# Performance work log

Measured on AMD Instinct MI355X. Metric: run time of the kernel, lower is better.

The kernel has to match this reference:

```python
import jax, jax.numpy as jnp
import numpy as np

D_MODEL = 1024
N_HEAD = 16
HEAD_DIM = D_MODEL // N_HEAD
D_INNER = (int(D_MODEL * 2.0) + 7) // 8 * 8  # 2048
EPS = 1e-6


def setup_inputs() -> dict:
    key = jax.random.key(0)
    ks = jax.random.split(key, 8)
    B, T = 2, 2048
    s = 0.02
    return {
        "x": jax.random.normal(ks[0], (B, T, D_MODEL), dtype=jnp.float32),
        "ln1_w": jnp.ones((D_MODEL,), jnp.float32),
        "ln2_w": jnp.ones((D_MODEL,), jnp.float32),
        "qkv_w": jax.random.normal(ks[1], (3 * D_MODEL, D_MODEL), jnp.float32) * s,
        "o_w": jax.random.normal(ks[2], (D_MODEL, D_MODEL), jnp.float32) * s,
        "gate_w": jax.random.normal(ks[3], (D_INNER, D_MODEL), jnp.float32) * s,
        "up_w": jax.random.normal(ks[4], (D_INNER, D_MODEL), jnp.float32) * s,
        "down_w": jax.random.normal(ks[5], (D_MODEL, D_INNER), jnp.float32) * s,
    }


def _rmsnorm(x, w):
    xf = x.astype(jnp.float32)
    rms = jax.lax.rsqrt(jnp.mean(xf * xf, axis=-1, keepdims=True) + EPS)
    return (xf * rms).astype(x.dtype) * w


def _attention(x, qkv_w, o_w):
    B, T, D = x.shape
    qkv = (x @ qkv_w.T).reshape(B, T, 3, N_HEAD, HEAD_DIM)
    q, k, v = qkv[:, :, 0], qkv[:, :, 1], qkv[:, :, 2]  # [B,T,H,hd]
    scale = 1.0 / np.sqrt(HEAD_DIM)
    att = jnp.einsum("bqhd,bkhd->bhqk", q, k) * scale
    causal = jnp.tril(jnp.ones((T, T), dtype=bool))
    att = jnp.where(causal[None, None], att, -jnp.inf)
    att = jax.nn.softmax(att, axis=-1)
    y = jnp.einsum("bhqk,bkhd->bqhd", att, v).reshape(B, T, D)
    return y @ o_w.T


def _ffn(x, gate_w, up_w, down_w):
    g = jax.nn.silu(x @ gate_w.T)
    u = x @ up_w.T
    return (g * u) @ down_w.T


def reference(x, ln1_w, ln2_w, qkv_w, o_w, gate_w, up_w, down_w):
    x = x + _attention(_rmsnorm(x, ln1_w), qkv_w, o_w)
    x = x + _ffn(_rmsnorm(x, ln2_w), gate_w, up_w, down_w)
    return x
```

## Files before the change

### kernel.cpp

```cpp
#include <hip/hip_runtime.h>
#include <hip/hip_bf16.h>
#include <cstdint>

typedef __hip_bfloat16 bf16;
typedef __attribute__((ext_vector_type(8))) short bf16x8;
typedef __attribute__((ext_vector_type(4))) float f32x4;
typedef __attribute__((ext_vector_type(4))) int i32x4;

#define T_SEQ 2048
#define DMODEL 1024
#define NHEAD 16
#define DHEAD 64
#define MROWS 4096

typedef const __attribute__((address_space(1))) void* gas_ptr;
typedef __attribute__((address_space(3))) void* las_ptr;

static __device__ __forceinline__ f32x4 mfma16(bf16x8 a, bf16x8 b, f32x4 c) {
  return __builtin_amdgcn_mfma_f32_16x16x32_bf16(a, b, c, 0, 0, 0);
}
static __device__ __forceinline__ void gload_lds16(const void* g, void* l) {
  __builtin_amdgcn_global_load_lds((gas_ptr)g, (las_ptr)l, 16, 0, 0);
}
static __device__ __forceinline__ float b2f(unsigned short u) {
  union { unsigned int i; float f; } x; x.i = ((unsigned int)u) << 16; return x.f;
}
static __device__ __forceinline__ unsigned short f2bu(float f) {
  __hip_bfloat16 h = __float2bfloat16(f);
  unsigned short u; __builtin_memcpy(&u, &h, 2); return u;
}

__global__ void f2b_k(const float* __restrict__ in, bf16* __restrict__ out, int n) {
  int idx = (blockIdx.x * blockDim.x + threadIdx.x) * 4;
  if (idx < n) {
    float4 v = *(const float4*)(in + idx);
    out[idx]     = __float2bfloat16(v.x);
    out[idx + 1] = __float2bfloat16(v.y);
    out[idx + 2] = __float2bfloat16(v.z);
    out[idx + 3] = __float2bfloat16(v.w);
  }
}

__global__ __launch_bounds__(256) void rms_k(const float* __restrict__ x,
                                             const float* __restrict__ w,
                                             bf16* __restrict__ out) {
  const int row = blockIdx.x;
  const int tid = threadIdx.x;
  const float4 v = ((const float4*)(x + (size_t)row * DMODEL))[tid];
  float ss = v.x * v.x + v.y * v.y + v.z * v.z + v.w * v.w;
#pragma unroll
  for (int off = 32; off; off >>= 1) ss += __shfl_xor(ss, off);
  __shared__ float red[4];
  if ((tid & 63) == 0) red[tid >> 6] = ss;
  __syncthreads();
  const float tot = red[0] + red[1] + red[2] + red[3];
  const float rinv = rsqrtf(tot * (1.f / DMODEL) + 1e-6f);
  const float4 wv = ((const float4*)w)[tid];
  bf16* o = out + (size_t)row * DMODEL + tid * 4;
  o[0] = __float2bfloat16(v.x * rinv * wv.x);
  o[1] = __float2bfloat16(v.y * rinv * wv.y);
  o[2] = __float2bfloat16(v.z * rinv * wv.z);
  o[3] = __float2bfloat16(v.w * rinv * wv.w);
}

template <int K, int EPI>
__global__ __launch_bounds__(256) void gemm_bt(const bf16* __restrict__ A,
                                               const bf16* __restrict__ Bw, int N,
                                               void* __restrict__ o0, void* __restrict__ o1,
                                               void* __restrict__ o2,
                                               const float* __restrict__ res) {
  __shared__ bf16 As[128 * 32];
  __shared__ bf16 Bs[128 * 32];
  const int bn0 = blockIdx.x * 128;
  const int bm0 = blockIdx.y * 128;
  const int tid = threadIdx.x;
  const int wave = tid >> 6, lane = tid & 63;
  const int wr = wave >> 1, wc = wave & 1;
  const int fr = lane & 15, g8 = (lane >> 4) * 8, r4 = (lane >> 4) * 4;
  const int srow = lane >> 2;
  const int scol = (lane & 3) * 8;

  const f32x4 fzero = {0.f, 0.f, 0.f, 0.f};
  f32x4 acc[4][4];
#pragma unroll
  for (int i = 0; i < 4; i++)
#pragma unroll
    for (int j = 0; j < 4; j++) acc[i][j] = fzero;

  const bf16* gA0 = A + (size_t)(bm0 + wave * 16 + srow) * K + scol;
  const bf16* gA1 = A + (size_t)(bm0 + (wave + 4) * 16 + srow) * K + scol;
  const bf16* gB0 = Bw + (size_t)(bn0 + wave * 16 + srow) * K + scol;
  const bf16* gB1 = Bw + (size_t)(bn0 + (wave + 4) * 16 + srow) * K + scol;

  for (int k0 = 0; k0 < K; k0 += 32) {
    gload_lds16(gA0 + k0, &As[wave * 512]);
    gload_lds16(gA1 + k0, &As[(wave + 4) * 512]);
    gload_lds16(gB0 + k0, &Bs[wave * 512]);
    gload_lds16(gB1 + k0, &Bs[(wave + 4) * 512]);
    __syncthreads();
    bf16x8 af[4], bfr[4];
#pragma unroll
    for (int mr = 0; mr < 4; mr++)
      af[mr] = *(const bf16x8*)&As[(wr * 64 + mr * 16 + fr) * 32 + g8];
#pragma unroll
    for (int nr = 0; nr < 4; nr++)
      bfr[nr] = *(const bf16x8*)&Bs[(wc * 64 + nr * 16 + fr) * 32 + g8];
#pragma unroll
    for (int mr = 0; mr < 4; mr++)
#pragma unroll
      for (int nr = 0; nr < 4; nr++)
        acc[mr][nr] = mfma16(af[mr], bfr[nr], acc[mr][nr]);
    __syncthreads();
  }

#pragma unroll
  for (int mr = 0; mr < 4; mr++) {
#pragma unroll
    for (int nr = 0; nr < 4; nr++) {
#pragma unroll
      for (int r = 0; r < 4; r++) {
        const int row = bm0 + wr * 64 + mr * 16 + r4 + r;
        const int col = bn0 + wc * 64 + nr * 16 + fr;
        const float vsum = acc[mr][nr][r];
        if (EPI == 0) {
          ((bf16*)o0)[(size_t)row * N + col] = __float2bfloat16(vsum);
        } else if (EPI == 1) {
          const int sel = col >> 10;
          const int n = col & 1023;
          const int h = n >> 6, d = n & 63;
          const int b = row >> 11, t = row & 2047;
          if (sel == 2) {
            ((bf16*)o2)[(((size_t)(b * NHEAD + h)) * DHEAD + d) * T_SEQ + t] =
                __float2bfloat16(vsum);
          } else {
            bf16* dst = (sel == 0) ? (bf16*)o0 : (bf16*)o1;
            dst[(((size_t)(b * NHEAD + h)) * T_SEQ + t) * DHEAD + d] = __float2bfloat16(vsum);
          }
        } else if (EPI == 2) {
          ((float*)o0)[(size_t)row * N + col] = res[(size_t)row * N + col] + vsum;
        } else {
          const int half = N >> 1;
          bf16* dst = (col < half) ? (bf16*)o0 : (bf16*)o1;
          const int c = (col < half) ? col : col - half;
          dst[(size_t)row * half + c] = __float2bfloat16(vsum);
        }
      }
    }
  }
}

__global__ __launch_bounds__(256) void attn_k(const bf16* __restrict__ qb,
                                              const bf16* __restrict__ kb,
                                              const bf16* __restrict__ vt,
                                              bf16* __restrict__ y) {
  const int wave = threadIdx.x >> 6, lane = threadIdx.x & 63;
  const int xcd = blockIdx.x & 7;
  const int j = blockIdx.x >> 3;
  const int bh = xcd * 4 + (j & 3);
  const int qt = 31 - (j >> 2);
  const int b = bh >> 4, h = bh & 15;
  const int fr = lane & 15, g8 = (lane >> 4) * 8, r4 = (lane >> 4) * 4;
  const int u = lane >> 4;
  const int src1 = fr + ((u & 1) << 5);
  const int src2 = src1 + 16;
  const bool hB = u >= 2;

  const bf16* qp = qb + (size_t)bh * T_SEQ * DHEAD;
  const bf16* kp = kb + (size_t)bh * T_SEQ * DHEAD;
  const bf16* vp = vt + (size_t)bh * DHEAD * T_SEQ;

  __shared__ char Ks[2][4096];
  __shared__ char Vs[2][4096];

  const int q0 = qt * 64 + wave * 16;
  const int kend = q0 + 16;
  const int qrow = q0 + fr;
  const int nb = 2 * qt + 2;

  const bf16x8 qf0 = *(const bf16x8*)(qp + (size_t)(q0 + fr) * DHEAD + g8);
  const bf16x8 qf1 = *(const bf16x8*)(qp + (size_t)(q0 + fr) * DHEAD + 32 + g8);

  const int krow_l = lane >> 3;
  const int kslot_l = (lane & 7) ^ krow_l;
  const int vrow_l = lane >> 2;
  const int vslot_l = (lane & 3) ^ ((lane >> 3) & 3);

  const int kswz = (fr & 7) << 4;
  const int koffA = fr * 128 + ((u * 16) ^ kswz);
  const int koffB = fr * 128 + (((4 + u) * 16) ^ kswz);
  const int vswz = ((fr >> 1) & 3) << 4;

  const f32x4 fzero = {0.f, 0.f, 0.f, 0.f};
  f32x4 acc[4];
  float lpart = 0.f;
#pragma unroll
  for (int nf = 0; nf < 4; nf++) acc[nf] = fzero;

  gload_lds16(kp + (size_t)(wave * 8 + krow_l) * DHEAD + kslot_l * 8,
              &Ks[0][wave * 1024]);
  gload_lds16(vp + (size_t)(wave * 16 + vrow_l) * T_SEQ + vslot_l * 8,
              &Vs[0][wave * 1024]);
  __syncthreads();

  for (int ts = 0; ts < nb; ++ts) {
    const int kt = ts * 32;
    const int buf = ts & 1;
    if (ts + 1 < nb) {
      const int kn = kt + 32;
      gload_lds16(kp + (size_t)(kn + wave * 8 + krow_l) * DHEAD + kslot_l * 8,
                  &Ks[buf ^ 1][wave * 1024]);
      gload_lds16(vp + (size_t)(wave * 16 + vrow_l) * T_SEQ + kn + vslot_l * 8,
                  &Vs[buf ^ 1][wave * 1024]);
    }
    if (kt < kend) {
      const char* KB = Ks[buf];
      const char* VB = Vs[buf];
      const bf16x8 kf0a = *(const bf16x8*)(KB + koffA);
      const bf16x8 kf0b = *(const bf16x8*)(KB + koffB);
      const bf16x8 kf1a = *(const bf16x8*)(KB + 2048 + koffA);
      const bf16x8 kf1b = *(const bf16x8*)(KB + 2048 + koffB);
      bf16x8 vf[4];
#pragma unroll
      for (int nf = 0; nf < 4; nf++)
        vf[nf] = *(const bf16x8*)(VB + (nf * 16 + fr) * 64 + ((u * 16) ^ vswz));

      f32x4 s0 = mfma16(kf0a, qf0, fzero);
      s0 = mfma16(kf0b, qf1, s0);
      f32x4 s1 = mfma16(kf1a, qf0, fzero);
      s1 = mfma16(kf1b, qf1, s1);

      float x0[4], x1[4];
      if (kt + 31 < q0) {
#pragma unroll
        for (int r = 0; r < 4; r++) {
          x0[r] = __expf(fminf(s0[r] * 0.125f, 30.f));
          x1[r] = __expf(fminf(s1[r] * 0.125f, 30.f));
          lpart += x0[r] + x1[r];
        }
      } else {
#pragma unroll
        for (int r = 0; r < 4; r++) {
          const int k0 = kt + r4 + r;
          const int k1 = k0 + 16;
          x0[r] = (k0 <= qrow) ? __expf(fminf(s0[r] * 0.125f, 30.f)) : 0.f;
          x1[r] = (k1 <= qrow) ? __expf(fminf(s1[r] * 0.125f, 30.f)) : 0.f;
          lpart += x0[r] + x1[r];
        }
      }

      const int A01 = (int)((unsigned)f2bu(x0[0]) | ((unsigned)f2bu(x0[1]) << 16));
      const int A23 = (int)((unsigned)f2bu(x0[2]) | ((unsigned)f2bu(x0[3]) << 16));
      const int B01 = (int)((unsigned)f2bu(x1[0]) | ((unsigned)f2bu(x1[1]) << 16));
      const int B23 = (int)((unsigned)f2bu(x1[2]) | ((unsigned)f2bu(x1[3]) << 16));

      const int t0a = __shfl(A01, src1), t0b = __shfl(B01, src1);
      const int t1a = __shfl(A23, src1), t1b = __shfl(B23, src1);
      const int t2a = __shfl(A01, src2), t2b = __shfl(B01, src2);
      const int t3a = __shfl(A23, src2), t3b = __shfl(B23, src2);
      i32x4 pw;
      pw[0] = hB ? t0b : t0a;
      pw[1] = hB ? t1b : t1a;
      pw[2] = hB ? t2b : t2a;
      pw[3] = hB ? t3b : t3a;
      const bf16x8 pb = __builtin_bit_cast(bf16x8, pw);

#pragma unroll
      for (int nf = 0; nf < 4; nf++) acc[nf] = mfma16(vf[nf], pb, acc[nf]);
    }
    __syncthreads();
  }

  lpart += __shfl_xor(lpart, 16);
  lpart += __shfl_xor(lpart, 32);
  const float inv = 1.f / lpart;

  const int t = q0 + fr;
  unsigned short* yb =
      (unsigned short*)(y + (((size_t)(b * T_SEQ + t)) * NHEAD + h) * DHEAD);
#pragma unroll
  for (int nf = 0; nf < 4; nf++) {
    ushort4 ov;
    ov.x = f2bu(acc[nf][0] * inv);
    ov.y = f2bu(acc[nf][1] * inv);
    ov.z = f2bu(acc[nf][2] * inv);
    ov.w = f2bu(acc[nf][3] * inv);
    *(ushort4*)(yb + nf * 16 + r4) = ov;
  }
}

__global__ void silumul_k(const bf16* __restrict__ g, const bf16* __restrict__ u,
                          bf16* __restrict__ o, int n) {
  const int idx = (blockIdx.x * blockDim.x + threadIdx.x) * 4;
  if (idx < n) {
    const ushort4 gv = *(const ushort4*)((const unsigned short*)g + idx);
    const ushort4 uv = *(const ushort4*)((const unsigned short*)u + idx);
    ushort4 ov;
    float a, s;
    a = b2f(gv.x); s = a / (1.f + __expf(-a)); ov.x = f2bu(s * b2f(uv.x));
    a = b2f(gv.y); s = a / (1.f + __expf(-a)); ov.y = f2bu(s * b2f(uv.y));
    a = b2f(gv.z); s = a / (1.f + __expf(-a)); ov.z = f2bu(s * b2f(uv.z));
    a = b2f(gv.w); s = a / (1.f + __expf(-a)); ov.w = f2bu(s * b2f(uv.w));
    *(ushort4*)((unsigned short*)o + idx) = ov;
  }
}

extern "C" void kernel_launch(void* const* d_in, const int* in_sizes, int n_in,
                              void* d_out, int out_size, void* d_ws, size_t ws_size,
                              hipStream_t stream) {
  const float* x     = (const float*)d_in[0];
  const float* ln1w  = (const float*)d_in[1];
  const float* ln2w  = (const float*)d_in[2];
  const float* qkvw  = (const float*)d_in[3];
  const float* ow    = (const float*)d_in[4];
  const float* gatew = (const float*)d_in[5];
  const float* upw   = (const float*)d_in[6];
  const float* downw = (const float*)d_in[7];

  uint8_t* ws = (uint8_t*)d_ws;
  bf16* WQKV = (bf16*)(ws + 0);
  bf16* WO   = (bf16*)(ws + 6291456);
  bf16* WG   = (bf16*)(ws + 8388608);
  bf16* WU   = (bf16*)(ws + 12582912);
  bf16* WD   = (bf16*)(ws + 16777216);
  bf16* H    = (bf16*)(ws + 20971520);
  bf16* Q    = (bf16*)(ws + 29360128);
  bf16* Kb   = (bf16*)(ws + 37748736);
  bf16* VT   = (bf16*)(ws + 46137344);
  bf16* Y    = (bf16*)(ws + 54525952);
  float* X2  = (float*)(ws + 62914560);
  bf16* G = (bf16*)(ws + 29360128);
  bf16* U = (bf16*)(ws + 46137344);

  f2b_k<<<3072, 256, 0, stream>>>(qkvw, WQKV, 3072 * 1024);
  f2b_k<<<1024, 256, 0, stream>>>(ow, WO, 1024 * 1024);
  f2b_k<<<2048, 256, 0, stream>>>(gatew, WG, 2048 * 1024);
  f2b_k<<<2048, 256, 0, stream>>>(upw, WU, 2048 * 1024);
  f2b_k<<<2048, 256, 0, stream>>>(downw, WD, 1024 * 2048);

  rms_k<<<MROWS, 256, 0, stream>>>(x, ln1w, H);
  gemm_bt<1024, 1><<<dim3(24, 32), 256, 0, stream>>>(H, WQKV, 3072, Q, Kb, VT, nullptr);
  attn_k<<<1024, 256, 0, stream>>>(Q, Kb, VT, Y);
  gemm_bt<1024, 2><<<dim3(8, 32), 256, 0, stream>>>(Y, WO, 1024, X2, nullptr, nullptr, x);

  rms_k<<<MROWS, 256, 0, stream>>>(X2, ln2w, H);
  gemm_bt<1024, 3><<<dim3(32, 32), 256, 0, stream>>>(H, WG, 4096, G, U, nullptr, nullptr);
  silumul_k<<<8192, 256, 0, stream>>>(G, U, G, 4096 * 2048);
  gemm_bt<2048, 2><<<dim3(8, 32), 256, 0, stream>>>(G, WD, 1024, (float*)d_out, nullptr, nullptr, X2);
}
```

Before: 254.6 us.

## Split long causal attention rows across two blocks and merge; fuse weight casts

Query tiles in the second half of the sequence now have their KV range split into two halves processed by separate blocks. Each block writes unnormalized partial outputs and row sums, and a new combine kernel adds and normalizes them. Short tiles still run in one block, which balances work across the grid and removes the long-tail blocks. The five weight conversion launches are also merged into one kernel. The cost is an extra launch and extra round-trips of partial results through global memory, and the partials are stored in bf16 before combining, which may add rounding error.

```diff
diff --git a/kernel.cpp b/kernel.cpp
--- a/kernel.cpp
+++ b/kernel.cpp
@@ -30,15 +30,24 @@
   unsigned short u; __builtin_memcpy(&u, &h, 2); return u;
 }
 
-__global__ void f2b_k(const float* __restrict__ in, bf16* __restrict__ out, int n) {
-  int idx = (blockIdx.x * blockDim.x + threadIdx.x) * 4;
-  if (idx < n) {
-    float4 v = *(const float4*)(in + idx);
-    out[idx]     = __float2bfloat16(v.x);
-    out[idx + 1] = __float2bfloat16(v.y);
-    out[idx + 2] = __float2bfloat16(v.z);
-    out[idx + 3] = __float2bfloat16(v.w);
-  }
+__global__ __launch_bounds__(256) void f2ball_k(const float* __restrict__ a,
+                                                const float* __restrict__ b,
+                                                const float* __restrict__ c,
+                                                const float* __restrict__ d,
+                                                const float* __restrict__ e,
+                                                bf16* __restrict__ out) {
+  const int idx = (blockIdx.x * 256 + threadIdx.x) * 4;
+  const float* src;
+  int off;
+  if (idx < 3145728)      { src = a; off = idx; }
+  else if (idx < 4194304) { src = b; off = idx - 3145728; }
+  else if (idx < 6291456) { src = c; off = idx - 4194304; }
+  else if (idx < 8388608) { src = d; off = idx - 6291456; }
+  else                    { src = e; off = idx - 8388608; }
+  const float4 v = *(const float4*)(src + off);
+  ushort4 ov;
+  ov.x = f2bu(v.x); ov.y = f2bu(v.y); ov.z = f2bu(v.z); ov.w = f2bu(v.w);
+  *(ushort4*)((unsigned short*)out + idx) = ov;
 }
 
 __global__ __launch_bounds__(256) void rms_k(const float* __restrict__ x,
@@ -152,12 +161,31 @@
 __global__ __launch_bounds__(256) void attn_k(const bf16* __restrict__ qb,
                                               const bf16* __restrict__ kb,
                                               const bf16* __restrict__ vt,
-                                              bf16* __restrict__ y) {
+                                              bf16* __restrict__ y,
+                                              unsigned short* __restrict__ pO,
+                                              float* __restrict__ pL) {
   const int wave = threadIdx.x >> 6, lane = threadIdx.x & 63;
-  const int xcd = blockIdx.x & 7;
-  const int j = blockIdx.x >> 3;
-  const int bh = xcd * 4 + (j & 3);
-  const int qt = 31 - (j >> 2);
+  const int bid = blockIdx.x;
+  int bh, qt, ks0, nb, heavy, hs;
+  if (bid < 1024) {
+    const int c = bid & 7, r = bid >> 3;
+    bh = c * 4 + (r & 3);
+    const int idx = r >> 2;
+    qt = 31 - (idx >> 1);
+    hs = idx & 1;
+    heavy = 1;
+    nb = qt + 1;
+    ks0 = hs * nb;
+  } else {
+    const int bd = bid - 1024;
+    const int c = bd & 7, r = bd >> 3;
+    bh = c * 4 + (r & 3);
+    qt = 15 - (r >> 2);
+    hs = 0;
+    heavy = 0;
+    nb = 2 * qt + 2;
+    ks0 = 0;
+  }
   const int b = bh >> 4, h = bh & 15;
   const int fr = lane & 15, g8 = (lane >> 4) * 8, r4 = (lane >> 4) * 4;
   const int u = lane >> 4;
@@ -175,7 +203,6 @@
   const int q0 = qt * 64 + wave * 16;
   const int kend = q0 + 16;
   const int qrow = q0 + fr;
-  const int nb = 2 * qt + 2;
 
   const bf16x8 qf0 = *(const bf16x8*)(qp + (size_t)(q0 + fr) * DHEAD + g8);
   const bf16x8 qf1 = *(const bf16x8*)(qp + (size_t)(q0 + fr) * DHEAD + 32 + g8);
@@ -196,14 +223,14 @@
 #pragma unroll
   for (int nf = 0; nf < 4; nf++) acc[nf] = fzero;
 
-  gload_lds16(kp + (size_t)(wave * 8 + krow_l) * DHEAD + kslot_l * 8,
+  gload_lds16(kp + (size_t)(ks0 * 32 + wave * 8 + krow_l) * DHEAD + kslot_l * 8,
               &Ks[0][wave * 1024]);
-  gload_lds16(vp + (size_t)(wave * 16 + vrow_l) * T_SEQ + vslot_l * 8,
+  gload_lds16(vp + (size_t)(wave * 16 + vrow_l) * T_SEQ + ks0 * 32 + vslot_l * 8,
               &Vs[0][wave * 1024]);
   __syncthreads();
 
   for (int ts = 0; ts < nb; ++ts) {
-    const int kt = ts * 32;
+    const int kt = (ks0 + ts) * 32;
     const int buf = ts & 1;
     if (ts + 1 < nb) {
       const int kn = kt + 32;
@@ -272,20 +299,55 @@
 
   lpart += __shfl_xor(lpart, 16);
   lpart += __shfl_xor(lpart, 32);
-  const float inv = 1.f / lpart;
-
-  const int t = q0 + fr;
-  unsigned short* yb =
-      (unsigned short*)(y + (((size_t)(b * T_SEQ + t)) * NHEAD + h) * DHEAD);
-#pragma unroll
-  for (int nf = 0; nf < 4; nf++) {
-    ushort4 ov;
-    ov.x = f2bu(acc[nf][0] * inv);
-    ov.y = f2bu(acc[nf][1] * inv);
-    ov.z = f2bu(acc[nf][2] * inv);
-    ov.w = f2bu(acc[nf][3] * inv);
-    *(ushort4*)(yb + nf * 16 + r4) = ov;
-  }
+
+  if (!heavy) {
+    const float inv = 1.f / lpart;
+    const int t = q0 + fr;
+    unsigned short* yb =
+        (unsigned short*)(y + (((size_t)(b * T_SEQ + t)) * NHEAD + h) * DHEAD);
+#pragma unroll
+    for (int nf = 0; nf < 4; nf++) {
+      ushort4 ov;
+      ov.x = f2bu(acc[nf][0] * inv);
+      ov.y = f2bu(acc[nf][1] * inv);
+      ov.z = f2bu(acc[nf][2] * inv);
+      ov.w = f2bu(acc[nf][3] * inv);
+      *(ushort4*)(yb + nf * 16 + r4) = ov;
+    }
+  } else {
+    const int tl = q0 - 1024 + fr;
+    unsigned short* po = pO + ((size_t)(hs * 32 + bh) * 1024 + tl) * DHEAD;
+#pragma unroll
+    for (int nf = 0; nf < 4; nf++) {
+      ushort4 ov;
+      ov.x = f2bu(acc[nf][0]);
+      ov.y = f2bu(acc[nf][1]);
+      ov.z = f2bu(acc[nf][2]);
+      ov.w = f2bu(acc[nf][3]);
+      *(ushort4*)(po + nf * 16 + r4) = ov;
+    }
+    if (lane < 16) pL[(size_t)(hs * 32 + bh) * 1024 + (q0 - 1024) + lane] = lpart;
+  }
+}
+
+__global__ __launch_bounds__(256) void comb_k(const unsigned short* __restrict__ pO,
+                                              const float* __restrict__ pL,
+                                              bf16* __restrict__ y) {
+  const int idx = blockIdx.x * 256 + threadIdx.x;
+  const int row = idx >> 4;
+  const int d0 = (idx & 15) * 4;
+  const int bh = row >> 10, tl = row & 1023;
+  const int b = bh >> 4, h = bh & 15;
+  const int t = 1024 + tl;
+  const float inv = 1.f / (pL[row] + pL[32768 + row]);
+  const ushort4 a = *(const ushort4*)(pO + (size_t)row * DHEAD + d0);
+  const ushort4 c = *(const ushort4*)(pO + (size_t)(32768 + row) * DHEAD + d0);
+  ushort4 ov;
+  ov.x = f2bu((b2f(a.x) + b2f(c.x)) * inv);
+  ov.y = f2bu((b2f(a.y) + b2f(c.y)) * inv);
+  ov.z = f2bu((b2f(a.z) + b2f(c.z)) * inv);
+  ov.w = f2bu((b2f(a.w) + b2f(c.w)) * inv);
+  *(ushort4*)((unsigned short*)y + (((size_t)(b * T_SEQ + t)) * NHEAD + h) * DHEAD + d0) = ov;
 }
 
 __global__ void silumul_k(const bf16* __restrict__ g, const bf16* __restrict__ u,
@@ -330,16 +392,15 @@
   float* X2  = (float*)(ws + 62914560);
   bf16* G = (bf16*)(ws + 29360128);
   bf16* U = (bf16*)(ws + 46137344);
-
-  f2b_k<<<3072, 256, 0, stream>>>(qkvw, WQKV, 3072 * 1024);
-  f2b_k<<<1024, 256, 0, stream>>>(ow, WO, 1024 * 1024);
-  f2b_k<<<2048, 256, 0, stream>>>(gatew, WG, 2048 * 1024);
-  f2b_k<<<2048, 256, 0, stream>>>(upw, WU, 2048 * 1024);
-  f2b_k<<<2048, 256, 0, stream>>>(downw, WD, 1024 * 2048);
+  unsigned short* pO = (unsigned short*)(ws + 62914560);
+  float* pL = (float*)(ws + 20971520);
+
+  f2ball_k<<<10240, 256, 0, stream>>>(qkvw, ow, gatew, upw, downw, (bf16*)ws);
 
   rms_k<<<MROWS, 256, 0, stream>>>(x, ln1w, H);
   gemm_bt<1024, 1><<<dim3(24, 32), 256, 0, stream>>>(H, WQKV, 3072, Q, Kb, VT, nullptr);
-  attn_k<<<1024, 256, 0, stream>>>(Q, Kb, VT, Y);
+  attn_k<<<1536, 256, 0, stream>>>(Q, Kb, VT, Y, pO, pL);
+  comb_k<<<2048, 256, 0, stream>>>(pO, pL, Y);
   gemm_bt<1024, 2><<<dim3(8, 32), 256, 0, stream>>>(Y, WO, 1024, X2, nullptr, nullptr, x);
 
   rms_k<<<MROWS, 256, 0, stream>>>(X2, ln2w, H);
```

Measured after the change: 242.8 us. 4.6% less time.
